# Performance work log

Hardware: AMD Instinct MI355X
Metric: run time of the kernel (lower is better)

The kernel has to match this reference:

```python
import jax, jax.numpy as jnp
import numpy as np

N_WIN = 232
T = 8
KERNEL = (2, 2, 2)
STRIDE = (2, 2, 2)
SLOPE = 25.0  # fast_sigmoid surrogate slope


@jax.custom_vjp
def spike(v):
    # heaviside(v) with fast-sigmoid surrogate gradient
    return (v > 0).astype(v.dtype)

def _spike_fwd(v):
    return spike(v), v

def _spike_bwd(v, g):
    return (g / (SLOPE * jnp.abs(v) + 1.0) ** 2,)

spike.defvjp(_spike_fwd, _spike_bwd)


def _avg_pool3d(x, kernel, stride):
    # x: (B, C, D, H, W), VALID pooling
    win = (1, 1) + tuple(kernel)
    st = (1, 1) + tuple(stride)
    s = jax.lax.reduce_window(x, 0.0, jax.lax.add, win, st, 'VALID')
    return s / float(np.prod(kernel))


def setup_inputs() -> dict:
    key = jax.random.key(0)
    ks = jax.random.split(key, 14)
    B, C, H, W = 64, 3, 32, 32
    input_dim, h0, h1, n_cls = 256, 256, 128, 6
    x = jax.random.normal(ks[0], (B, C, N_WIN, H, W), jnp.float32)
    W_in = jax.random.normal(ks[1], (h0, input_dim), jnp.float32) * 0.05
    b_in = jnp.zeros((h0,), jnp.float32)
    W_hid = jax.random.normal(ks[2], (h1, h0), jnp.float32) * 0.05
    b_hid = jnp.zeros((h1,), jnp.float32)
    in_feat = C * h1 * 14  # C * hidden[1] * D'
    W_out = jax.random.normal(ks[3], (n_cls, in_feat), jnp.float32) * 0.05
    b_out = jnp.zeros((n_cls,), jnp.float32)
    beta_in = jax.random.uniform(ks[4], (h0,), jnp.float32)
    thr_in = jax.random.uniform(ks[5], (h0,), jnp.float32)
    beta_hid = jax.random.uniform(ks[6], (h1,), jnp.float32)
    thr_hid = jax.random.uniform(ks[7], (h1,), jnp.float32)
    beta_out = jax.random.uniform(ks[8], (n_cls,), jnp.float32)
    return dict(x=x, W_in=W_in, b_in=b_in, W_hid=W_hid, b_hid=b_hid,
                W_out=W_out, b_out=b_out, beta_in=beta_in, thr_in=thr_in,
                beta_hid=beta_hid, thr_hid=thr_hid, beta_out=beta_out)


def _lif(mem, cur, beta, thr):
    # snntorch Leaky, reset-by-subtract; reset uses detached prev-mem spike
    reset = jax.lax.stop_gradient((mem > thr).astype(mem.dtype))
    mem = jnp.clip(beta, 0.0, 1.0) * mem + cur - reset * thr
    spk = spike(mem - thr)
    return spk, mem


def reference(x, W_in, b_in, W_hid, b_hid, W_out, b_out,
              beta_in, thr_in, beta_hid, thr_hid, beta_out):
    B, C, _, H, W = x.shape
    chunk = N_WIN // T  # 29
    # split depth into T chunks: (T, B, C, chunk, H, W)
    xt = x.reshape(B, C, T, chunk, H, W).transpose(2, 0, 1, 3, 4, 5)
    pooled = jax.vmap(lambda v: _avg_pool3d(v, KERNEL, STRIDE))(xt)  # (T,B,C,D',H',W')
    _, _, _, Dp, Hp, Wp = pooled.shape
    pr = pooled.reshape(T, B, C * Dp, Hp * Wp)
    # fc_in applied to all timesteps at once (recurrence-free)
    cur_in_all = jnp.einsum('tbnf,hf->tbnh', pr, W_in) + b_in  # (T,B,N,h0)

    h0 = W_in.shape[0]
    h1 = W_hid.shape[0]
    n_cls = W_out.shape[0]
    N = C * Dp
    mem_in0 = jnp.zeros((B, N, h0), x.dtype)
    mem_hid0 = jnp.zeros((B, N, h1), x.dtype)
    mem_out0 = jnp.zeros((B, n_cls), x.dtype)

    def step(carry, cur_in):
        mem_in, mem_hid, mem_out = carry
        spk_in, mem_in = _lif(mem_in, cur_in, beta_in, thr_in)
        cur_hid = jnp.einsum('bnh,gh->bng', spk_in, W_hid) + b_hid
        spk_hid, mem_hid = _lif(mem_hid, cur_hid, beta_hid, thr_hid)
        flat = spk_hid.reshape(spk_hid.shape[0], -1)  # (B, N*h1)
        cur_out = flat @ W_out.T + b_out
        spk_out, mem_out = _lif(mem_out, cur_out, beta_out, jnp.float32(1.0))
        return (mem_in, mem_hid, mem_out), spk_out

    _, spk_rec = jax.lax.scan(step, (mem_in0, mem_hid0, mem_out0), cur_in_all)
    return spk_rec  # (T, B, n_classes)
```

## Files before the change

kernel.cpp:

```cpp
#include <hip/hip_runtime.h>

#define T_STEPS 8
#define NROW    42
#define BN      2688
#define H0      256
#define H1      128
#define NCLS    6
#define KFLAT   5376

#define SW(r)   ((r) + ((r) >> 5) * 4)
#define LDR     140

__global__ __launch_bounds__(256) void pool_kernel(const float* __restrict__ x,
                                                   float* __restrict__ pr) {
    int idx = blockIdx.x * 256 + threadIdx.x;
    int f   = idx & 255;
    int wp  = f & 15, hp = f >> 4;
    int rest = idx >> 8;
    int dp = rest % 14;
    int r2 = rest / 14;
    int c  = r2 % 3;
    int r3 = r2 / 3;
    int b  = r3 & 63;
    int t  = r3 >> 6;
    const float* base = x + ((long)b * 712704 + (long)c * 237568
                          + (long)(t * 29 + 2 * dp) * 1024
                          + (2 * hp) * 32 + 2 * wp);
    float2 v0 = *(const float2*)(base);
    float2 v1 = *(const float2*)(base + 32);
    float2 v2 = *(const float2*)(base + 1024);
    float2 v3 = *(const float2*)(base + 1056);
    float s = v0.x + v0.y + v1.x + v1.y + v2.x + v2.y + v3.x + v3.y;
    int m = t * BN + b * NROW + c * 14 + dp;
    pr[(long)m * 256 + f] = s * 0.125f;
}

__global__ __launch_bounds__(256, 4) void gemm_abt(const float* __restrict__ A,
                                                   const float* __restrict__ B,
                                                   const float* __restrict__ bias,
                                                   float* __restrict__ C,
                                                   int N, int K) {
    __shared__ float At[16 * LDR];
    __shared__ float Bt[16 * LDR];
    int tid = threadIdx.x;
    int m0 = blockIdx.y * 128, n0 = blockIdx.x * 128;

    int sr = tid >> 1, sq = tid & 1;
    int scol = SW(sr);
    const float* Ap = A + (long)(m0 + sr) * K + sq * 8;
    const float* Bp = B + (long)(n0 + sr) * K + sq * 8;

    int tm = tid & 15, tn = tid >> 4;
    int ca = SW(tm * 8);
    int cb = SW(tn * 8);

    float acc[8][8] = {};

    for (int k0 = 0; k0 < K; k0 += 16) {
        float4 a0 = *(const float4*)(Ap + k0);
        float4 a1 = *(const float4*)(Ap + k0 + 4);
        float4 b0 = *(const float4*)(Bp + k0);
        float4 b1 = *(const float4*)(Bp + k0 + 4);
        __syncthreads();
        int kb = sq * 8;
        At[(kb + 0) * LDR + scol] = a0.x; At[(kb + 1) * LDR + scol] = a0.y;
        At[(kb + 2) * LDR + scol] = a0.z; At[(kb + 3) * LDR + scol] = a0.w;
        At[(kb + 4) * LDR + scol] = a1.x; At[(kb + 5) * LDR + scol] = a1.y;
        At[(kb + 6) * LDR + scol] = a1.z; At[(kb + 7) * LDR + scol] = a1.w;
        Bt[(kb + 0) * LDR + scol] = b0.x; Bt[(kb + 1) * LDR + scol] = b0.y;
        Bt[(kb + 2) * LDR + scol] = b0.z; Bt[(kb + 3) * LDR + scol] = b0.w;
        Bt[(kb + 4) * LDR + scol] = b1.x; Bt[(kb + 5) * LDR + scol] = b1.y;
        Bt[(kb + 6) * LDR + scol] = b1.z; Bt[(kb + 7) * LDR + scol] = b1.w;
        __syncthreads();
#pragma unroll
        for (int k = 0; k < 16; ++k) {
            float4 av0 = *(const float4*)&At[k * LDR + ca];
            float4 av1 = *(const float4*)&At[k * LDR + ca + 4];
            float4 bv0 = *(const float4*)&Bt[k * LDR + cb];
            float4 bv1 = *(const float4*)&Bt[k * LDR + cb + 4];
            float am[8] = {av0.x, av0.y, av0.z, av0.w, av1.x, av1.y, av1.z, av1.w};
            float bn_[8] = {bv0.x, bv0.y, bv0.z, bv0.w, bv1.x, bv1.y, bv1.z, bv1.w};
#pragma unroll
            for (int i = 0; i < 8; ++i)
#pragma unroll
                for (int j = 0; j < 8; ++j)
                    acc[i][j] = fmaf(am[i], bn_[j], acc[i][j]);
        }
    }

#pragma unroll
    for (int i = 0; i < 8; ++i) {
        int row = m0 + tm * 8 + i;
        int col = n0 + tn * 8;
        float4 o0, o1;
        o0.x = acc[i][0] + bias[col + 0];
        o0.y = acc[i][1] + bias[col + 1];
        o0.z = acc[i][2] + bias[col + 2];
        o0.w = acc[i][3] + bias[col + 3];
        o1.x = acc[i][4] + bias[col + 4];
        o1.y = acc[i][5] + bias[col + 5];
        o1.z = acc[i][6] + bias[col + 6];
        o1.w = acc[i][7] + bias[col + 7];
        *(float4*)&C[(long)row * N + col]     = o0;
        *(float4*)&C[(long)row * N + col + 4] = o1;
    }
}

__global__ __launch_bounds__(256) void lif_kernel(const float* __restrict__ cur_all,
                                                  const float* __restrict__ beta,
                                                  const float* __restrict__ thr,
                                                  float* __restrict__ spk_all,
                                                  int F) {
    int j = blockIdx.x * 256 + threadIdx.x;
    int h = j & (F - 1);
    float be = fminf(fmaxf(beta[h], 0.f), 1.f);
    float th = thr[h];
    float mem = 0.f;
    long stride = (long)BN * F;
#pragma unroll
    for (int t = 0; t < T_STEPS; ++t) {
        float cur = cur_all[t * stride + j];
        float reset = (mem > th) ? th : 0.f;
        mem = be * mem + cur - reset;
        spk_all[t * stride + j] = ((mem - th) > 0.f) ? 1.f : 0.f;
    }
}

__global__ __launch_bounds__(256) void out_gemm(const float* __restrict__ spkh,
                                                const float* __restrict__ W_out,
                                                const float* __restrict__ b_out,
                                                float* __restrict__ cur_out) {
    __shared__ float part[256][8];
    int row = blockIdx.x;
    int tid = threadIdx.x;
    const float* a = spkh + (long)row * KFLAT;
    float acc[6] = {0.f, 0.f, 0.f, 0.f, 0.f, 0.f};
    for (int j = tid; j < KFLAT; j += 256) {
        float s = a[j];
#pragma unroll
        for (int c = 0; c < 6; ++c)
            acc[c] = fmaf(s, W_out[c * KFLAT + j], acc[c]);
    }
#pragma unroll
    for (int c = 0; c < 6; ++c) part[tid][c] = acc[c];
    __syncthreads();
    for (int off = 128; off > 0; off >>= 1) {
        if (tid < off) {
#pragma unroll
            for (int c = 0; c < 6; ++c) part[tid][c] += part[tid + off][c];
        }
        __syncthreads();
    }
    if (tid < 6) cur_out[row * 6 + tid] = part[0][tid] + b_out[tid];
}

__global__ void lif_out_kernel(const float* __restrict__ cur_out,
                               const float* __restrict__ beta_out,
                               float* __restrict__ out) {
    int j = threadIdx.x;
    if (j >= 384) return;
    int cls = j % 6;
    float be = fminf(fmaxf(beta_out[cls], 0.f), 1.f);
    float mem = 0.f;
#pragma unroll
    for (int t = 0; t < T_STEPS; ++t) {
        float cur = cur_out[t * 384 + j];
        float reset = (mem > 1.f) ? 1.f : 0.f;
        mem = be * mem + cur - reset;
        out[t * 384 + j] = ((mem - 1.f) > 0.f) ? 1.f : 0.f;
    }
}

extern "C" void kernel_launch(void* const* d_in, const int* in_sizes, int n_in,
                              void* d_out, int out_size, void* d_ws, size_t ws_size,
                              hipStream_t stream) {
    (void)in_sizes; (void)n_in; (void)out_size; (void)ws_size;
    const float* x        = (const float*)d_in[0];
    const float* W_in     = (const float*)d_in[1];
    const float* b_in     = (const float*)d_in[2];
    const float* W_hid    = (const float*)d_in[3];
    const float* b_hid    = (const float*)d_in[4];
    const float* W_out    = (const float*)d_in[5];
    const float* b_out    = (const float*)d_in[6];
    const float* beta_in  = (const float*)d_in[7];
    const float* thr_in   = (const float*)d_in[8];
    const float* beta_hid = (const float*)d_in[9];
    const float* thr_hid  = (const float*)d_in[10];
    const float* beta_out = (const float*)d_in[11];
    float* out = (float*)d_out;

    float* buf0 = (float*)d_ws;
    float* buf1 = buf0 + 5505024;
    float* curo = buf1 + 5505024;

    pool_kernel<<<21504, 256, 0, stream>>>(x, buf0);
    gemm_abt<<<dim3(2, 168), 256, 0, stream>>>(buf0, W_in, b_in, buf1, 256, 256);
    lif_kernel<<<2688, 256, 0, stream>>>(buf1, beta_in, thr_in, buf0, 256);
    gemm_abt<<<dim3(1, 168), 256, 0, stream>>>(buf0, W_hid, b_hid, buf1, 128, 256);
    lif_kernel<<<1344, 256, 0, stream>>>(buf1, beta_hid, thr_hid, buf0, 128);
    out_gemm<<<512, 256, 0, stream>>>(buf0, W_out, b_out, curo);
    lif_out_kernel<<<1, 384, 0, stream>>>(curo, beta_out, out);
}
```

Measured before the change: 402.1 us.

## Fuse LIF recurrence into GEMM epilogue by reordering rows time-innermost

The pooled rows are now laid out with the timestep as the fastest row index, so each thread's 8 accumulator rows cover the 8 timesteps of one neuron position. This lets the GEMM epilogue run the LIF recurrence in registers and write spikes directly, removing both standalone LIF kernels and their round trips of the current tensors through global memory. The output GEMM gathers spikes with strided indexing to match the new layout. Launch bounds drop to 2 waves-per-SIMD hint, and the out_gemm reads become less contiguous.

```diff
diff --git a/kernel.cpp b/kernel.cpp
--- a/kernel.cpp
+++ b/kernel.cpp
@@ -7,6 +7,7 @@
 #define H1      128
 #define NCLS    6
 #define KFLAT   5376
+
 
 #define SW(r)   ((r) + ((r) >> 5) * 4)
 #define LDR     140
@@ -31,14 +32,16 @@
     float2 v2 = *(const float2*)(base + 1024);
     float2 v3 = *(const float2*)(base + 1056);
     float s = v0.x + v0.y + v1.x + v1.y + v2.x + v2.y + v3.x + v3.y;
-    int m = t * BN + b * NROW + c * 14 + dp;
+    int m = (b * NROW + c * 14 + dp) * 8 + t;
     pr[(long)m * 256 + f] = s * 0.125f;
 }
 
-__global__ __launch_bounds__(256, 4) void gemm_abt(const float* __restrict__ A,
+__global__ __launch_bounds__(256, 2) void gemm_lif(const float* __restrict__ A,
                                                    const float* __restrict__ B,
                                                    const float* __restrict__ bias,
-                                                   float* __restrict__ C,
+                                                   const float* __restrict__ beta,
+                                                   const float* __restrict__ thr,
+                                                   float* __restrict__ spk,
                                                    int N, int K) {
     __shared__ float At[16 * LDR];
     __shared__ float Bt[16 * LDR];
@@ -89,40 +92,29 @@
     }
 
 #pragma unroll
-    for (int i = 0; i < 8; ++i) {
-        int row = m0 + tm * 8 + i;
-        int col = n0 + tn * 8;
-        float4 o0, o1;
-        o0.x = acc[i][0] + bias[col + 0];
-        o0.y = acc[i][1] + bias[col + 1];
-        o0.z = acc[i][2] + bias[col + 2];
-        o0.w = acc[i][3] + bias[col + 3];
-        o1.x = acc[i][4] + bias[col + 4];
-        o1.y = acc[i][5] + bias[col + 5];
-        o1.z = acc[i][6] + bias[col + 6];
-        o1.w = acc[i][7] + bias[col + 7];
-        *(float4*)&C[(long)row * N + col]     = o0;
-        *(float4*)&C[(long)row * N + col + 4] = o1;
+    for (int c = 0; c < 8; ++c) {
+        int h = n0 + tn * 8 + c;
+        float be = fminf(fmaxf(beta[h], 0.f), 1.f);
+        float th = thr[h];
+        float bi = bias[h];
+        float mem = 0.f;
+#pragma unroll
+        for (int t = 0; t < T_STEPS; ++t) {
+            float cur = acc[t][c] + bi;
+            float reset = (mem > th) ? th : 0.f;
+            mem = be * mem + cur - reset;
+            acc[t][c] = ((mem - th) > 0.f) ? 1.f : 0.f;
+        }
     }
-}
-
-__global__ __launch_bounds__(256) void lif_kernel(const float* __restrict__ cur_all,
-                                                  const float* __restrict__ beta,
-                                                  const float* __restrict__ thr,
-                                                  float* __restrict__ spk_all,
-                                                  int F) {
-    int j = blockIdx.x * 256 + threadIdx.x;
-    int h = j & (F - 1);
-    float be = fminf(fmaxf(beta[h], 0.f), 1.f);
-    float th = thr[h];
-    float mem = 0.f;
-    long stride = (long)BN * F;
+    int rbase = m0 + tm * 8;
 #pragma unroll
     for (int t = 0; t < T_STEPS; ++t) {
-        float cur = cur_all[t * stride + j];
-        float reset = (mem > th) ? th : 0.f;
-        mem = be * mem + cur - reset;
-        spk_all[t * stride + j] = ((mem - th) > 0.f) ? 1.f : 0.f;
+        long row = rbase + t;
+        int col = n0 + tn * 8;
+        float4 o0 = {acc[t][0], acc[t][1], acc[t][2], acc[t][3]};
+        float4 o1 = {acc[t][4], acc[t][5], acc[t][6], acc[t][7]};
+        *(float4*)&spk[row * N + col]     = o0;
+        *(float4*)&spk[row * N + col + 4] = o1;
     }
 }
 
@@ -132,11 +124,12 @@
                                                 float* __restrict__ cur_out) {
     __shared__ float part[256][8];
     int row = blockIdx.x;
+    int t = row >> 6, b = row & 63;
     int tid = threadIdx.x;
-    const float* a = spkh + (long)row * KFLAT;
     float acc[6] = {0.f, 0.f, 0.f, 0.f, 0.f, 0.f};
     for (int j = tid; j < KFLAT; j += 256) {
-        float s = a[j];
+        int n = j >> 7, h = j & 127;
+        float s = spkh[((long)(b * NROW + n) * 8 + t) * 128 + h];
 #pragma unroll
         for (int c = 0; c < 6; ++c)
             acc[c] = fmaf(s, W_out[c * KFLAT + j], acc[c]);
@@ -194,10 +187,10 @@
     float* curo = buf1 + 5505024;
 
     pool_kernel<<<21504, 256, 0, stream>>>(x, buf0);
-    gemm_abt<<<dim3(2, 168), 256, 0, stream>>>(buf0, W_in, b_in, buf1, 256, 256);
-    lif_kernel<<<2688, 256, 0, stream>>>(buf1, beta_in, thr_in, buf0, 256);
-    gemm_abt<<<dim3(1, 168), 256, 0, stream>>>(buf0, W_hid, b_hid, buf1, 128, 256);
-    lif_kernel<<<1344, 256, 0, stream>>>(buf1, beta_hid, thr_hid, buf0, 128);
+    gemm_lif<<<dim3(2, 168), 256, 0, stream>>>(buf0, W_in, b_in, beta_in, thr_in,
+                                               buf1, 256, 256);
+    gemm_lif<<<dim3(1, 168), 256, 0, stream>>>(buf1, W_hid, b_hid, beta_hid, thr_hid,
+                                               buf0, 128, 256);
     out_gemm<<<512, 256, 0, stream>>>(buf0, W_out, b_out, curo);
     lif_out_kernel<<<1, 384, 0, stream>>>(curo, beta_out, out);
 }
```

Result: faster. 388.0 us (-3.5%).
